# Optimization experiments

Measured on AMD Instinct MI355X. Metric: run time of the kernel, lower is better.

## Reference

```python
import jax, jax.numpy as jnp
import numpy as np

NUM_LEVELS = 16
BASE_RES = 16
LOG2_HASH = 19
HASH_SIZE = 1 << LOG2_HASH
FEAT = 32
RES = 128
N = 262144
HASH_MASK = np.uint32(HASH_SIZE - 1)
P1 = np.uint32(2654435761)
P2 = np.uint32(805459861)


def setup_inputs() -> dict:
    key = jax.random.key(0)
    ks = jax.random.split(key, 8)
    return {
        "xyz": jax.random.uniform(ks[0], (N, 3), dtype=jnp.float32),
        "feature_grids": jax.random.normal(ks[1], (NUM_LEVELS, HASH_SIZE, FEAT), dtype=jnp.float32) * 0.1,
        "density_grid": jax.random.normal(ks[2], (RES, RES, RES), dtype=jnp.float32) * 0.1,
        "W1": jax.random.normal(ks[3], (NUM_LEVELS * FEAT, 64), dtype=jnp.float32) * 0.04,
        "b1": jnp.zeros((64,), dtype=jnp.float32),
        "W2": jax.random.normal(ks[4], (64, 64), dtype=jnp.float32) * 0.12,
        "b2": jnp.zeros((64,), dtype=jnp.float32),
        "W3": jax.random.normal(ks[5], (64, 3), dtype=jnp.float32) * 0.12,
        "b3": jnp.zeros((3,), dtype=jnp.float32),
    }


def _get_features(xyz, feature_grids):
    # grid_res per level: 16 * 2^l, l = 0..15 (max 524288, fits fp32/uint32)
    res = (BASE_RES * (2 ** jnp.arange(NUM_LEVELS, dtype=jnp.float32).astype(jnp.int32))).astype(jnp.float32)
    # [L, N, 3] integer voxel coords; xyz in [0,1) so trunc == floor == torch .long()
    idx = (xyz[None, :, :] * res[:, None, None]).astype(jnp.uint32)
    # spatial hash in uint32: low 19 bits identical to torch's int64 (x*1 ^ y*p1 ^ z*p2) % 2^19
    h = (idx[..., 0] ^ (idx[..., 1] * P1) ^ (idx[..., 2] * P2)) & HASH_MASK  # [L, N]
    # gather per level from its own table, then concat over levels (level-major last dim)
    feats = jnp.take_along_axis(feature_grids, h[..., None].astype(jnp.int32), axis=1)  # [L, N, F]
    return jnp.moveaxis(feats, 0, 1).reshape(xyz.shape[0], NUM_LEVELS * FEAT)  # [N, L*F]


def reference(xyz, feature_grids, density_grid, W1, b1, W2, b2, W3, b3):
    features = _get_features(xyz, feature_grids)           # [N, 512]
    density = jax.nn.sigmoid(density_grid)                 # [128,128,128]
    h = jax.nn.relu(features @ W1 + b1)
    h = jax.nn.relu(h @ W2 + b2)
    color = jax.nn.sigmoid(h @ W3 + b3)                    # [N, 3]
    return (density, color)
```

## Files before the change

### kernel.cpp

```cpp
#include <hip/hip_runtime.h>
#include <hip/hip_bf16.h>
#include <cstdint>

#define HASH_SIZE (1u<<19)
#define NPTS 262144
#define DENS_N 2097152

typedef unsigned short u16;
typedef u16 u16x8 __attribute__((ext_vector_type(8)));
typedef __bf16 bf16x8 __attribute__((ext_vector_type(8)));
typedef float f32x4 __attribute__((ext_vector_type(4)));

__device__ __forceinline__ u16 f2bf(float f){
  uint32_t u = __builtin_bit_cast(uint32_t, f);
  u += 0x7fffu + ((u>>16)&1u);
  return (u16)(u>>16);
}
__device__ __forceinline__ float bf2f(u16 s){
  uint32_t u = ((uint32_t)s)<<16;
  return __builtin_bit_cast(float, u);
}

__global__ void prep_weights(const float* __restrict__ W1, const float* __restrict__ W2,
                             u16* __restrict__ W1T, u16* __restrict__ W2T){
  int t = blockIdx.x*blockDim.x + threadIdx.x;
  int stride = gridDim.x*blockDim.x;
  for (int i=t; i<64*512; i+=stride){ int o=i>>9, k=i&511; W1T[i] = f2bf(W1[k*64+o]); }
  for (int i=t; i<64*64;  i+=stride){ int o=i>>6, k=i&63;  W2T[i] = f2bf(W2[k*64+o]); }
}

__global__ void density_sigmoid(const float4* __restrict__ in, float4* __restrict__ out){
  int i = blockIdx.x*blockDim.x + threadIdx.x;
  float4 v = in[i];
  v.x = 1.f/(1.f+__expf(-v.x));
  v.y = 1.f/(1.f+__expf(-v.y));
  v.z = 1.f/(1.f+__expf(-v.z));
  v.w = 1.f/(1.f+__expf(-v.w));
  out[i] = v;
}

__global__ void __launch_bounds__(512) fused_mlp(
    const float* __restrict__ xyz, const float* __restrict__ fg,
    const u16* __restrict__ W1T, const u16* __restrict__ W2T,
    const float* __restrict__ b1, const float* __restrict__ b2,
    const float* __restrict__ W3, const float* __restrict__ b3,
    float* __restrict__ color)
{
  __shared__ u16 w1s[64*512];
  __shared__ u16 w2s[64*64];
  __shared__ u16 hbuf[8][16*64];

  const int t = threadIdx.x;
  const int wave = t >> 6;
  const int lane = t & 63;
  const int p  = lane & 15;
  const int kg = lane >> 4;
  const int gp = (blockIdx.x << 7) + (wave << 4) + p;

  const float x = xyz[gp*3+0];
  const float y = xyz[gp*3+1];
  const float z = xyz[gp*3+2];
  float4 a0[16], a1[16];
  #pragma unroll
  for (int s=0; s<16; ++s){
    const float resf = (float)(16 << s);
    uint32_t ix = (uint32_t)(x*resf);
    uint32_t iy = (uint32_t)(y*resf);
    uint32_t iz = (uint32_t)(z*resf);
    uint32_t h = (ix ^ (iy*2654435761u) ^ (iz*805459861u)) & (HASH_SIZE-1u);
    const float* ap = fg + (size_t)((((uint32_t)s<<19) | h) * 32u) + (kg<<3);
    a0[s] = *(const float4*)ap;
    a1[s] = *(const float4*)(ap+4);
  }

  #pragma unroll
  for (int i=0; i<8; ++i){
    int g = t + (i<<9);
    int col = g >> 6, gr = g & 63;
    u16x8 v = *(const u16x8*)(W1T + (g<<3));
    *(u16x8*)(w1s + (col<<9) + (((gr) ^ (col&7))<<3)) = v;
  }
  {
    int g = t;
    int col = g >> 3, gr = g & 7;
    u16x8 v = *(const u16x8*)(W2T + (g<<3));
    *(u16x8*)(w2s + (col<<6) + (((gr) ^ (col&7))<<3)) = v;
  }
  __syncthreads();

  f32x4 acc[4];
  #pragma unroll
  for (int tt=0; tt<4; ++tt) acc[tt] = (f32x4){0.f,0.f,0.f,0.f};

  #pragma unroll
  for (int s=0; s<16; ++s){
    bf16x8 ab = { (__bf16)a0[s].x, (__bf16)a0[s].y, (__bf16)a0[s].z, (__bf16)a0[s].w,
                  (__bf16)a1[s].x, (__bf16)a1[s].y, (__bf16)a1[s].z, (__bf16)a1[s].w };
    #pragma unroll
    for (int tt=0; tt<4; ++tt){
      const int col = (lane&15) + (tt<<4);
      u16x8 bu = *(const u16x8*)(w1s + (col<<9) + ((((s<<2)+kg) ^ (col&7))<<3));
      acc[tt] = __builtin_amdgcn_mfma_f32_16x16x32_bf16(
          ab, __builtin_bit_cast(bf16x8, bu), acc[tt], 0,0,0);
    }
  }
  #pragma unroll
  for (int tt=0; tt<4; ++tt){
    const int col = (lane&15) + (tt<<4);
    const float bias = b1[col];
    #pragma unroll
    for (int r=0; r<4; ++r){
      const int row = (kg<<2) + r;
      float v = acc[tt][r] + bias;
      v = v > 0.f ? v : 0.f;
      hbuf[wave][(row*64 + col) ^ ((row&7)<<3)] = f2bf(v);
    }
  }

  f32x4 acc2[4];
  #pragma unroll
  for (int tt=0; tt<4; ++tt) acc2[tt] = (f32x4){0.f,0.f,0.f,0.f};

  #pragma unroll
  for (int kc=0; kc<2; ++kc){
    const int aidx = (p*64 + kc*32 + kg*8) ^ ((p&7)<<3);
    u16x8 au = *(const u16x8*)(&hbuf[wave][aidx]);
    bf16x8 ab = __builtin_bit_cast(bf16x8, au);
    #pragma unroll
    for (int tt=0; tt<4; ++tt){
      const int col = (lane&15) + (tt<<4);
      u16x8 bu = *(const u16x8*)(w2s + (col<<6) + ((((kc<<2)+kg) ^ (col&7))<<3));
      acc2[tt] = __builtin_amdgcn_mfma_f32_16x16x32_bf16(
          ab, __builtin_bit_cast(bf16x8, bu), acc2[tt], 0,0,0);
    }
  }
  #pragma unroll
  for (int tt=0; tt<4; ++tt){
    const int col = (lane&15) + (tt<<4);
    const float bias = b2[col];
    #pragma unroll
    for (int r=0; r<4; ++r){
      const int row = (kg<<2) + r;
      float v = acc2[tt][r] + bias;
      v = v > 0.f ? v : 0.f;
      hbuf[wave][(row*64 + col) ^ ((row&7)<<3)] = f2bf(v);
    }
  }

  if (lane < 48){
    const int pp = lane / 3, c = lane % 3;
    float sum = b3[c];
    #pragma unroll
    for (int o=0; o<64; ++o){
      sum += bf2f(hbuf[wave][(pp*64+o) ^ ((pp&7)<<3)]) * W3[o*3+c];
    }
    const int gpp = (blockIdx.x << 7) + (wave << 4) + pp;
    color[(size_t)gpp*3 + c] = 1.f/(1.f+__expf(-sum));
  }
}

extern "C" void kernel_launch(void* const* d_in, const int* in_sizes, int n_in,
                              void* d_out, int out_size, void* d_ws, size_t ws_size,
                              hipStream_t stream){
  const float* xyz  = (const float*)d_in[0];
  const float* fg   = (const float*)d_in[1];
  const float* dens = (const float*)d_in[2];
  const float* W1   = (const float*)d_in[3];
  const float* b1   = (const float*)d_in[4];
  const float* W2   = (const float*)d_in[5];
  const float* b2   = (const float*)d_in[6];
  const float* W3   = (const float*)d_in[7];
  const float* b3   = (const float*)d_in[8];
  float* out = (float*)d_out;

  u16* W1T = (u16*)d_ws;
  u16* W2T = W1T + 64*512;

  hipLaunchKernelGGL(prep_weights, dim3(64), dim3(256), 0, stream, W1, W2, W1T, W2T);
  hipLaunchKernelGGL(density_sigmoid, dim3(DENS_N/1024), dim3(256), 0, stream,
                     (const float4*)dens, (float4*)out);
  hipLaunchKernelGGL(fused_mlp, dim3(NPTS/128), dim3(512), 0, stream,
                     xyz, fg, W1T, W2T, b1, b2, W3, b3, out + DENS_N);
}
```

Measured before the change: 129.6 us.

## Make MLP kernel persistent with software-pipelined hash-grid gathers

Launches 256 blocks, and each one loops over 8 batches of 128 points. The W1/W2 shared-memory staging is paid once per block instead of once per 128 points. The hash-table gathers for the next batch are issued in two halves, interleaved with the MFMA work on the current batch, and sched_barriers hold that ordering so gather latency can be hidden. In exchange there are fewer waves in flight for latency hiding (256 blocks on a 256-CU device) and higher register pressure from the double-buffered feature registers.

```diff
diff --git a/kernel.cpp b/kernel.cpp
--- a/kernel.cpp
+++ b/kernel.cpp
@@ -55,107 +55,138 @@
   const int lane = t & 63;
   const int p  = lane & 15;
   const int kg = lane >> 4;
-  const int gp = (blockIdx.x << 7) + (wave << 4) + p;
-
-  const float x = xyz[gp*3+0];
-  const float y = xyz[gp*3+1];
-  const float z = xyz[gp*3+2];
-  float4 a0[16], a1[16];
-  #pragma unroll
-  for (int s=0; s<16; ++s){
-    const float resf = (float)(16 << s);
-    uint32_t ix = (uint32_t)(x*resf);
-    uint32_t iy = (uint32_t)(y*resf);
-    uint32_t iz = (uint32_t)(z*resf);
-    uint32_t h = (ix ^ (iy*2654435761u) ^ (iz*805459861u)) & (HASH_SIZE-1u);
-    const float* ap = fg + (size_t)((((uint32_t)s<<19) | h) * 32u) + (kg<<3);
-    a0[s] = *(const float4*)ap;
-    a1[s] = *(const float4*)(ap+4);
-  }
+  const int base = (blockIdx.x << 10) + (wave << 4) + p;
+
+  auto issue8 = [&](float xx, float yy, float zz, int s0, float4* f0, float4* f1){
+    #pragma unroll
+    for (int j=0; j<8; ++j){
+      const int s = s0 + j;
+      const float resf = (float)(16 << s);
+      uint32_t ix = (uint32_t)(xx*resf);
+      uint32_t iy = (uint32_t)(yy*resf);
+      uint32_t iz = (uint32_t)(zz*resf);
+      uint32_t h = (ix ^ (iy*2654435761u) ^ (iz*805459861u)) & (HASH_SIZE-1u);
+      const float* ap = fg + (size_t)((((uint32_t)s<<19) | h) * 32u) + (kg<<3);
+      f0[j] = *(const float4*)ap;
+      f1[j] = *(const float4*)(ap+4);
+    }
+  };
+  auto drain8 = [&](int s0, const float4* f0, const float4* f1, f32x4* acc){
+    #pragma unroll
+    for (int j=0; j<8; ++j){
+      const int s = s0 + j;
+      bf16x8 ab = { (__bf16)f0[j].x, (__bf16)f0[j].y, (__bf16)f0[j].z, (__bf16)f0[j].w,
+                    (__bf16)f1[j].x, (__bf16)f1[j].y, (__bf16)f1[j].z, (__bf16)f1[j].w };
+      #pragma unroll
+      for (int tt=0; tt<4; ++tt){
+        const int col = (lane&15) + (tt<<4);
+        u16x8 bu = *(const u16x8*)(w1s + (col<<9) + ((((s<<2)+kg) ^ (col&7))<<3));
+        acc[tt] = __builtin_amdgcn_mfma_f32_16x16x32_bf16(
+            ab, __builtin_bit_cast(bf16x8, bu), acc[tt], 0,0,0);
+      }
+    }
+  };
+
+  float4 fa0[8], fa1[8], fb0[8], fb1[8];
+  {
+    const float x = xyz[base*3+0], y = xyz[base*3+1], z = xyz[base*3+2];
+    issue8(x, y, z, 0, fa0, fa1);
+    issue8(x, y, z, 8, fb0, fb1);
+  }
+  __builtin_amdgcn_sched_barrier(0);
 
   #pragma unroll
   for (int i=0; i<8; ++i){
     int g = t + (i<<9);
     int col = g >> 6, gr = g & 63;
     u16x8 v = *(const u16x8*)(W1T + (g<<3));
-    *(u16x8*)(w1s + (col<<9) + (((gr) ^ (col&7))<<3)) = v;
+    *(u16x8*)(w1s + (col<<9) + ((gr ^ (col&7))<<3)) = v;
   }
   {
     int g = t;
     int col = g >> 3, gr = g & 7;
     u16x8 v = *(const u16x8*)(W2T + (g<<3));
-    *(u16x8*)(w2s + (col<<6) + (((gr) ^ (col&7))<<3)) = v;
+    *(u16x8*)(w2s + (col<<6) + ((gr ^ (col&7))<<3)) = v;
+  }
+  float bias1[4], bias2[4];
+  #pragma unroll
+  for (int tt=0; tt<4; ++tt){
+    bias1[tt] = b1[(lane&15) + (tt<<4)];
+    bias2[tt] = b2[(lane&15) + (tt<<4)];
   }
   __syncthreads();
 
-  f32x4 acc[4];
-  #pragma unroll
-  for (int tt=0; tt<4; ++tt) acc[tt] = (f32x4){0.f,0.f,0.f,0.f};
-
-  #pragma unroll
-  for (int s=0; s<16; ++s){
-    bf16x8 ab = { (__bf16)a0[s].x, (__bf16)a0[s].y, (__bf16)a0[s].z, (__bf16)a0[s].w,
-                  (__bf16)a1[s].x, (__bf16)a1[s].y, (__bf16)a1[s].z, (__bf16)a1[s].w };
+  #pragma unroll 1
+  for (int b=0; b<8; ++b){
+    float xn=0.f, yn=0.f, zn=0.f;
+    if (b < 7){
+      const int gpn = base + ((b+1)<<7);
+      xn = xyz[gpn*3+0]; yn = xyz[gpn*3+1]; zn = xyz[gpn*3+2];
+    }
+
+    f32x4 acc[4];
+    #pragma unroll
+    for (int tt=0; tt<4; ++tt) acc[tt] = (f32x4){0.f,0.f,0.f,0.f};
+
+    drain8(0, fa0, fa1, acc);
+    __builtin_amdgcn_sched_barrier(0);
+    if (b < 7) issue8(xn, yn, zn, 0, fa0, fa1);
+    __builtin_amdgcn_sched_barrier(0);
+    drain8(8, fb0, fb1, acc);
+    __builtin_amdgcn_sched_barrier(0);
+    if (b < 7) issue8(xn, yn, zn, 8, fb0, fb1);
+    __builtin_amdgcn_sched_barrier(0);
+
     #pragma unroll
     for (int tt=0; tt<4; ++tt){
       const int col = (lane&15) + (tt<<4);
-      u16x8 bu = *(const u16x8*)(w1s + (col<<9) + ((((s<<2)+kg) ^ (col&7))<<3));
-      acc[tt] = __builtin_amdgcn_mfma_f32_16x16x32_bf16(
-          ab, __builtin_bit_cast(bf16x8, bu), acc[tt], 0,0,0);
-    }
-  }
-  #pragma unroll
-  for (int tt=0; tt<4; ++tt){
-    const int col = (lane&15) + (tt<<4);
-    const float bias = b1[col];
-    #pragma unroll
-    for (int r=0; r<4; ++r){
-      const int row = (kg<<2) + r;
-      float v = acc[tt][r] + bias;
-      v = v > 0.f ? v : 0.f;
-      hbuf[wave][(row*64 + col) ^ ((row&7)<<3)] = f2bf(v);
-    }
-  }
-
-  f32x4 acc2[4];
-  #pragma unroll
-  for (int tt=0; tt<4; ++tt) acc2[tt] = (f32x4){0.f,0.f,0.f,0.f};
-
-  #pragma unroll
-  for (int kc=0; kc<2; ++kc){
-    const int aidx = (p*64 + kc*32 + kg*8) ^ ((p&7)<<3);
-    u16x8 au = *(const u16x8*)(&hbuf[wave][aidx]);
-    bf16x8 ab = __builtin_bit_cast(bf16x8, au);
+      #pragma unroll
+      for (int r=0; r<4; ++r){
+        const int row = (kg<<2) + r;
+        float v = acc[tt][r] + bias1[tt];
+        v = v > 0.f ? v : 0.f;
+        hbuf[wave][(row*64 + col) ^ ((row&7)<<3)] = f2bf(v);
+      }
+    }
+
+    f32x4 acc2[4];
+    #pragma unroll
+    for (int tt=0; tt<4; ++tt) acc2[tt] = (f32x4){0.f,0.f,0.f,0.f};
+    #pragma unroll
+    for (int kc=0; kc<2; ++kc){
+      const int aidx = (p*64 + kc*32 + kg*8) ^ ((p&7)<<3);
+      u16x8 au = *(const u16x8*)(&hbuf[wave][aidx]);
+      bf16x8 ab = __builtin_bit_cast(bf16x8, au);
+      #pragma unroll
+      for (int tt=0; tt<4; ++tt){
+        const int col = (lane&15) + (tt<<4);
+        u16x8 bu = *(const u16x8*)(w2s + (col<<6) + ((((kc<<2)+kg) ^ (col&7))<<3));
+        acc2[tt] = __builtin_amdgcn_mfma_f32_16x16x32_bf16(
+            ab, __builtin_bit_cast(bf16x8, bu), acc2[tt], 0,0,0);
+      }
+    }
     #pragma unroll
     for (int tt=0; tt<4; ++tt){
       const int col = (lane&15) + (tt<<4);
-      u16x8 bu = *(const u16x8*)(w2s + (col<<6) + ((((kc<<2)+kg) ^ (col&7))<<3));
-      acc2[tt] = __builtin_amdgcn_mfma_f32_16x16x32_bf16(
-          ab, __builtin_bit_cast(bf16x8, bu), acc2[tt], 0,0,0);
-    }
-  }
-  #pragma unroll
-  for (int tt=0; tt<4; ++tt){
-    const int col = (lane&15) + (tt<<4);
-    const float bias = b2[col];
-    #pragma unroll
-    for (int r=0; r<4; ++r){
-      const int row = (kg<<2) + r;
-      float v = acc2[tt][r] + bias;
-      v = v > 0.f ? v : 0.f;
-      hbuf[wave][(row*64 + col) ^ ((row&7)<<3)] = f2bf(v);
-    }
-  }
-
-  if (lane < 48){
-    const int pp = lane / 3, c = lane % 3;
-    float sum = b3[c];
-    #pragma unroll
-    for (int o=0; o<64; ++o){
-      sum += bf2f(hbuf[wave][(pp*64+o) ^ ((pp&7)<<3)]) * W3[o*3+c];
-    }
-    const int gpp = (blockIdx.x << 7) + (wave << 4) + pp;
-    color[(size_t)gpp*3 + c] = 1.f/(1.f+__expf(-sum));
+      #pragma unroll
+      for (int r=0; r<4; ++r){
+        const int row = (kg<<2) + r;
+        float v = acc2[tt][r] + bias2[tt];
+        v = v > 0.f ? v : 0.f;
+        hbuf[wave][(row*64 + col) ^ ((row&7)<<3)] = f2bf(v);
+      }
+    }
+
+    if (lane < 48){
+      const int pp = lane / 3, c = lane % 3;
+      float sum = b3[c];
+      #pragma unroll
+      for (int o=0; o<64; ++o){
+        sum += bf2f(hbuf[wave][(pp*64+o) ^ ((pp&7)<<3)]) * W3[o*3+c];
+      }
+      const int gpp = (blockIdx.x << 10) + (b<<7) + (wave << 4) + pp;
+      color[(size_t)gpp*3 + c] = 1.f/(1.f+__expf(-sum));
+    }
   }
 }
 
@@ -179,6 +210,6 @@
   hipLaunchKernelGGL(prep_weights, dim3(64), dim3(256), 0, stream, W1, W2, W1T, W2T);
   hipLaunchKernelGGL(density_sigmoid, dim3(DENS_N/1024), dim3(256), 0, stream,
                      (const float4*)dens, (float4*)out);
-  hipLaunchKernelGGL(fused_mlp, dim3(NPTS/128), dim3(512), 0, stream,
+  hipLaunchKernelGGL(fused_mlp, dim3(256), dim3(512), 0, stream,
                      xyz, fg, W1T, W2T, b1, b2, W3, b3, out + DENS_N);
 }
```

Result: slower. 170.7 us (+31.7%).
